# Performance work log

Hardware: AMD Instinct MI355X
Metric: run time of the kernel (lower is better)

## Reference

```python
import heapq
import jax, jax.numpy as jnp
import numpy as np

NB_CLASSES = 50257
INPUT_DIM = 512
BATCH = 1024
NB_REQ = 8


def build_huffman(nb_classes):
    """Replicates Huffmax.build: huffman tree over equal frequencies,
    codes padded with 0, paths padded with root node id."""
    heap = [(1, i, i) for i in range(nb_classes)]  # (freq, tiebreak, payload)
    heapq.heapify(heap)
    node_id = 0
    tiebreak = nb_classes
    while len(heap) > 1:
        f1, _, left = heapq.heappop(heap)
        f2, _, right = heapq.heappop(heap)
        heapq.heappush(heap, (f1 + f2, tiebreak, ('n', node_id, left, right)))
        node_id += 1
        tiebreak += 1
    root = heap[0][2]
    total_nodes = node_id  # = nb_classes - 1
    root_id = root[1]
    codes, paths = {}, {}
    stack = [(root, [], [])]
    while stack:
        node, code, path = stack.pop()
        if isinstance(node, tuple):
            _, nid, l, r = node
            stack.append((l, code + [0], path + [nid]))
            stack.append((r, code + [1], path + [nid]))
        else:
            codes[node] = code
            paths[node] = path
    max_depth = max(len(c) for c in codes.values())
    code_arr = np.zeros((nb_classes, max_depth), np.float32)
    path_arr = np.full((nb_classes, max_depth), root_id, np.int32)
    for c in range(nb_classes):
        code_arr[c, :len(codes[c])] = codes[c]
        path_arr[c, :len(paths[c])] = paths[c]
    return code_arr, path_arr, total_nodes


def setup_inputs() -> dict:
    key = jax.random.key(0)
    k1, k2, k3 = jax.random.split(key, 3)
    code_arr, path_arr, total_nodes = build_huffman(NB_CLASSES)
    input_vector = jax.random.normal(k1, (BATCH, INPUT_DIM), dtype=jnp.float32)
    target_classes = jax.random.randint(k2, (BATCH, NB_REQ), 0, NB_CLASSES, dtype=jnp.int32)
    # glorot-ish scaled node weights (original W is (total_nodes, input_dim, 1))
    W = jax.random.normal(k3, (total_nodes, INPUT_DIM), dtype=jnp.float32) * (1.0 / np.sqrt(INPUT_DIM))
    b = jnp.zeros((total_nodes,), dtype=jnp.float32)
    return {
        'input_vector': input_vector,
        'target_classes': target_classes,
        'W': W,
        'b': b,
        'class_paths': jnp.asarray(path_arr),
        'huffman_codes': jnp.asarray(code_arr),
    }


def reference(input_vector, target_classes, W, b, class_paths, huffman_codes):
    # req_nodes: (B, R, D) node ids along huffman path for each requested class
    req_nodes = class_paths[target_classes]
    # req_W: (B, R, D, I) gathered node weight rows; y = x . W_node + b_node
    req_W = W[req_nodes]
    y = jnp.einsum('bi,brdi->brd', input_vector, req_W) + b[req_nodes]
    y = jax.nn.sigmoid(y)
    codes = huffman_codes[target_classes]  # (B, R, D) in {0,1} (0-padded)
    # factor = y if code==0 else (1-y); product along the path
    return jnp.prod(codes + y - 2.0 * codes * y, axis=-1)
```

## Files before the change

### kernel.cpp

```cpp
#include <hip/hip_runtime.h>
#include <math.h>

template<int CTRL, int ROW_MASK>
__device__ __forceinline__ float dpp_add(float v) {
    const int s = __builtin_amdgcn_update_dpp(0, __float_as_int(v),
                                              CTRL, ROW_MASK, 0xf, false);
    return v + __int_as_float(s);
}

__device__ __forceinline__ float wave_sum63(float v) {
    v = dpp_add<0x111, 0xf>(v);
    v = dpp_add<0x112, 0xf>(v);
    v = dpp_add<0x114, 0xf>(v);
    v = dpp_add<0x118, 0xf>(v);
    v = dpp_add<0x142, 0xa>(v);
    v = dpp_add<0x143, 0xc>(v);
    return v;
}

__device__ __forceinline__ float readlane_f(float v, int l) {
    return __int_as_float(__builtin_amdgcn_readlane(__float_as_int(v), l));
}

__global__ __launch_bounds__(256, 4)
void huff_half(const float* __restrict__ x, const int* __restrict__ tgt,
               const float* __restrict__ W, const float* __restrict__ bias,
               const int* __restrict__ paths, const float* __restrict__ codes,
               float* __restrict__ out, int R, int I)
{
    __shared__ float qsh[2][2];
    const int lane = threadIdx.x & 63;
    const int w    = threadIdx.x >> 6;
    const int pi   = w >> 1;
    const int h    = w & 1;
    const int p    = blockIdx.x * 2 + pi;
    const int b    = p / R;

    const float4* xrow = reinterpret_cast<const float4*>(x + (size_t)b * I);
    const float4 xa = xrow[lane];
    const float4 xb = xrow[lane + 64];

    const int c     = tgt[p];
    const int dglob = h * 8 + (lane & 7);
    const int   nd = paths[(size_t)c * 16 + dglob];
    const float cd = codes[(size_t)c * 16 + dglob];
    const float sd = 1.0f - 2.0f * cd;
    const float bv = bias[nd];

    float acc[8];
    #pragma unroll
    for (int d = 0; d < 8; ++d) {
        const int nid = __builtin_amdgcn_readlane(nd, d);
        const float4* wr = reinterpret_cast<const float4*>(W + (size_t)nid * I);
        const float4 wa = wr[lane];
        const float4 wb = wr[lane + 64];
        acc[d] = xa.x * wa.x + xa.y * wa.y + xa.z * wa.z + xa.w * wa.w
               + xb.x * wb.x + xb.y * wb.y + xb.z * wb.z + xb.w * wb.w;
    }

    #pragma unroll
    for (int d = 0; d < 8; ++d) acc[d] = wave_sum63(acc[d]);

    float q = 1.0f;
    #pragma unroll
    for (int d = 0; d < 8; ++d) {
        const float tot = readlane_f(acc[d], 63);
        const float bb  = readlane_f(bv, d);
        const float ss  = readlane_f(sd, d);
        q *= 1.0f + __expf(-ss * (tot + bb));
    }
    if (lane == 0) qsh[pi][h] = q;
    __syncthreads();
    if (h == 0 && lane == 0) out[p] = 1.0f / (qsh[pi][0] * qsh[pi][1]);
}

__global__ __launch_bounds__(256)
void huff_kernel_gen(const float* __restrict__ x, const int* __restrict__ tgt,
                     const float* __restrict__ W, const float* __restrict__ bias,
                     const int* __restrict__ paths, const float* __restrict__ codes,
                     float* __restrict__ out, int R, int I, int D, int npairs)
{
    const int lane = threadIdx.x & 63;
    const int p = blockIdx.x * 4 + (threadIdx.x >> 6);
    if (p >= npairs) return;
    const int b = p / R;
    const float4* xrow = reinterpret_cast<const float4*>(x + (size_t)b * I);
    const float4 xa = xrow[lane];
    const float4 xb = xrow[lane + 64];
    const int c = tgt[p];
    float q = 1.0f;
    for (int d = 0; d < D; ++d) {
        const int node = paths[(size_t)c * D + d];
        const float4* wr = reinterpret_cast<const float4*>(W + (size_t)node * I);
        const float4 wa = wr[lane];
        const float4 wb = wr[lane + 64];
        float acc = xa.x * wa.x + xa.y * wa.y + xa.z * wa.z + xa.w * wa.w
                  + xb.x * wb.x + xb.y * wb.y + xb.z * wb.z + xb.w * wb.w;
        #pragma unroll
        for (int off = 32; off; off >>= 1) acc += __shfl_xor(acc, off, 64);
        const float t = acc + bias[node];
        const float s = 1.0f - 2.0f * codes[(size_t)c * D + d];
        q *= 1.0f + __expf(-s * t);
    }
    if (lane == 0) out[p] = 1.0f / q;
}

extern "C" void kernel_launch(void* const* d_in, const int* in_sizes, int n_in,
                              void* d_out, int out_size, void* d_ws, size_t ws_size,
                              hipStream_t stream) {
    const float* x     = (const float*)d_in[0];
    const int*   tgt   = (const int*)  d_in[1];
    const float* W     = (const float*)d_in[2];
    const float* bias  = (const float*)d_in[3];
    const int*   paths = (const int*)  d_in[4];
    const float* codes = (const float*)d_in[5];
    float* out = (float*)d_out;

    const int N = in_sizes[3];
    const int C = N + 1;
    const int I = in_sizes[2] / N;
    const int B = in_sizes[0] / I;
    const int R = in_sizes[1] / B;
    const int D = in_sizes[4] / C;

    const int npairs = B * R;

    if (D == 16 && I == 512 && (npairs & 1) == 0) {
        huff_half<<<npairs / 2, 256, 0, stream>>>(x, tgt, W, bias, paths, codes,
                                                  out, R, I);
    } else {
        const int grid = (npairs + 3) / 4;
        huff_kernel_gen<<<grid, 256, 0, stream>>>(x, tgt, W, bias, paths, codes,
                                                  out, R, I, D, npairs);
    }
}
```

Before: 24.12 us.

## Precompute top-tree node logits densely, gather remaining path nodes per pair

Adds a dense pre-pass that computes logits for the top 128 Huffman nodes (highest ids, near the root) for every batch row into workspace. The per-pair kernel then reads the first seven shared path nodes from that table and only gathers and dots the remaining nine weight rows. A fallback loop handles pairs whose first seven nodes are not all in the table. This trades redundant per-pair gathers of heavily shared upper-tree rows for an extra launch, a workspace round trip, and reliance on the node-id layout of the tree construction.

```diff
diff --git a/kernel.cpp b/kernel.cpp
--- a/kernel.cpp
+++ b/kernel.cpp
@@ -1,13 +1,18 @@
 #include <hip/hip_runtime.h>
 #include <math.h>
 
+#define TOPM 128
+
 template<int CTRL, int ROW_MASK>
 __device__ __forceinline__ float dpp_add(float v) {
-    const int s = __builtin_amdgcn_update_dpp(0, __float_as_int(v),
-                                              CTRL, ROW_MASK, 0xf, false);
+    const int s = __builtin_amdgcn_update_dpp(0, __float_as_int(v), CTRL, ROW_MASK, 0xf, false);
     return v + __int_as_float(s);
 }
-
+template<int CTRL, int ROW_MASK>
+__device__ __forceinline__ float dpp_mul(float v) {
+    const int s = __builtin_amdgcn_update_dpp(0x3f800000, __float_as_int(v), CTRL, ROW_MASK, 0xf, false);
+    return v * __int_as_float(s);
+}
 __device__ __forceinline__ float wave_sum63(float v) {
     v = dpp_add<0x111, 0xf>(v);
     v = dpp_add<0x112, 0xf>(v);
@@ -17,61 +22,134 @@
     v = dpp_add<0x143, 0xc>(v);
     return v;
 }
-
+__device__ __forceinline__ float wave_prod63(float v) {
+    v = dpp_mul<0x111, 0xf>(v);
+    v = dpp_mul<0x112, 0xf>(v);
+    v = dpp_mul<0x114, 0xf>(v);
+    v = dpp_mul<0x118, 0xf>(v);
+    v = dpp_mul<0x142, 0xa>(v);
+    v = dpp_mul<0x143, 0xc>(v);
+    return v;
+}
 __device__ __forceinline__ float readlane_f(float v, int l) {
     return __int_as_float(__builtin_amdgcn_readlane(__float_as_int(v), l));
 }
-
-__global__ __launch_bounds__(256, 4)
-void huff_half(const float* __restrict__ x, const int* __restrict__ tgt,
-               const float* __restrict__ W, const float* __restrict__ bias,
-               const int* __restrict__ paths, const float* __restrict__ codes,
-               float* __restrict__ out, int R, int I)
+__device__ __forceinline__ float dot8(float4 a, float4 b, float4 c, float4 d) {
+    return a.x*b.x + a.y*b.y + a.z*b.z + a.w*b.w
+         + c.x*d.x + c.y*d.y + c.z*d.z + c.w*d.w;
+}
+
+__global__ __launch_bounds__(256)
+void dense_top(const float* __restrict__ x, const float* __restrict__ W,
+               const float* __restrict__ bias, float* __restrict__ ytop, int N)
 {
-    __shared__ float qsh[2][2];
     const int lane = threadIdx.x & 63;
-    const int w    = threadIdx.x >> 6;
-    const int pi   = w >> 1;
-    const int h    = w & 1;
-    const int p    = blockIdx.x * 2 + pi;
-    const int b    = p / R;
-
-    const float4* xrow = reinterpret_cast<const float4*>(x + (size_t)b * I);
-    const float4 xa = xrow[lane];
-    const float4 xb = xrow[lane + 64];
-
-    const int c     = tgt[p];
-    const int dglob = h * 8 + (lane & 7);
-    const int   nd = paths[(size_t)c * 16 + dglob];
-    const float cd = codes[(size_t)c * 16 + dglob];
+    const int wi = blockIdx.x * 4 + (threadIdx.x >> 6);
+    const int bchunk = wi >> 4;
+    const int jg = wi & 15;
+    const int tb = N - TOPM;
+
+    float4 wa[8], wb[8];
+    #pragma unroll
+    for (int r = 0; r < 8; ++r) {
+        const float4* wr = reinterpret_cast<const float4*>(W + (size_t)(tb + jg*8 + r) * 512);
+        wa[r] = wr[lane]; wb[r] = wr[lane + 64];
+    }
+    float bb[8];
+    #pragma unroll
+    for (int r = 0; r < 8; ++r) bb[r] = bias[tb + jg*8 + r];
+
+    for (int bl = 0; bl < 16; ++bl) {
+        const int b = bchunk * 16 + bl;
+        const float4* xr = reinterpret_cast<const float4*>(x + (size_t)b * 512);
+        const float4 xa = xr[lane], xb = xr[lane + 64];
+        float acc[8];
+        #pragma unroll
+        for (int r = 0; r < 8; ++r) acc[r] = dot8(xa, wa[r], xb, wb[r]);
+        #pragma unroll
+        for (int r = 0; r < 8; ++r) acc[r] = wave_sum63(acc[r]);
+        float tv = 0.0f;
+        #pragma unroll
+        for (int r = 0; r < 8; ++r) {
+            const float tot = readlane_f(acc[r], 63) + bb[r];
+            tv = (lane == r) ? tot : tv;
+        }
+        if (lane < 8) ytop[(size_t)b * TOPM + jg * 8 + lane] = tv;
+    }
+}
+
+__global__ __launch_bounds__(256)
+void huff_table(const float* __restrict__ x, const int* __restrict__ tgt,
+                const float* __restrict__ W, const float* __restrict__ bias,
+                const int* __restrict__ paths, const float* __restrict__ codes,
+                const float* __restrict__ ytop, float* __restrict__ out,
+                int R, int N)
+{
+    const int lane = threadIdx.x & 63;
+    const int p = blockIdx.x * 4 + (threadIdx.x >> 6);
+    const int b = p / R;
+    const int tb = N - TOPM;
+
+    const float4* xr = reinterpret_cast<const float4*>(x + (size_t)b * 512);
+    const float4 xa = xr[lane], xb = xr[lane + 64];
+
+    const int c = tgt[p];
+    const int dd = (lane < 16) ? lane : 15;
+    const int   nd = paths[(size_t)c * 16 + dd];
+    const float cd = codes[(size_t)c * 16 + dd];
     const float sd = 1.0f - 2.0f * cd;
     const float bv = bias[nd];
 
-    float acc[8];
-    #pragma unroll
-    for (int d = 0; d < 8; ++d) {
-        const int nid = __builtin_amdgcn_readlane(nd, d);
-        const float4* wr = reinterpret_cast<const float4*>(W + (size_t)nid * I);
-        const float4 wa = wr[lane];
-        const float4 wb = wr[lane + 64];
-        acc[d] = xa.x * wa.x + xa.y * wa.y + xa.z * wa.z + xa.w * wa.w
-               + xb.x * wb.x + xb.y * wb.y + xb.z * wb.z + xb.w * wb.w;
-    }
-
-    #pragma unroll
-    for (int d = 0; d < 8; ++d) acc[d] = wave_sum63(acc[d]);
-
-    float q = 1.0f;
-    #pragma unroll
-    for (int d = 0; d < 8; ++d) {
-        const float tot = readlane_f(acc[d], 63);
-        const float bb  = readlane_f(bv, d);
-        const float ss  = readlane_f(sd, d);
-        q *= 1.0f + __expf(-ss * (tot + bb));
-    }
-    if (lane == 0) qsh[pi][h] = q;
-    __syncthreads();
-    if (h == 0 && lane == 0) out[p] = 1.0f / (qsh[pi][0] * qsh[pi][1]);
+    const unsigned long long gmask = __ballot(lane < 16 && nd < tb);
+
+    if ((gmask & 0x7Full) == 0) {
+        float tval = 0.0f;
+        if (lane < 7) tval = ytop[(size_t)b * TOPM + (nd - tb)];
+
+        float4 wA[9], wB[9];
+        #pragma unroll
+        for (int i = 0; i < 9; ++i) {
+            const int snid = __builtin_amdgcn_readlane(nd, 7 + i);
+            const float4* wr = reinterpret_cast<const float4*>(W + (size_t)snid * 512);
+            wA[i] = wr[lane]; wB[i] = wr[lane + 64];
+        }
+        float acc[9];
+        #pragma unroll
+        for (int i = 0; i < 9; ++i) acc[i] = dot8(xa, wA[i], xb, wB[i]);
+        #pragma unroll
+        for (int i = 0; i < 9; ++i) acc[i] = wave_sum63(acc[i]);
+
+        float f = 1.0f;
+        if (lane < 7) f = 1.0f + __expf(-sd * tval);
+        f = wave_prod63(f);
+        float q = readlane_f(f, 63);
+
+        #pragma unroll
+        for (int i = 0; i < 9; ++i) {
+            const float tot = readlane_f(acc[i], 63) + readlane_f(bv, 7 + i);
+            const float ss  = readlane_f(sd, 7 + i);
+            q *= 1.0f + __expf(-ss * tot);
+        }
+        if (lane == 0) out[p] = 1.0f / q;
+    } else {
+        float q = 1.0f;
+        for (int d = 0; d < 16; ++d) {
+            const int snid = __builtin_amdgcn_readlane(nd, d);
+            const float ss = readlane_f(sd, d);
+            float t;
+            if (snid >= tb) {
+                t = ytop[(size_t)b * TOPM + (snid - tb)];
+            } else {
+                const float4* wr = reinterpret_cast<const float4*>(W + (size_t)snid * 512);
+                const float4 wva = wr[lane], wvb = wr[lane + 64];
+                float a = dot8(xa, wva, xb, wvb);
+                a = wave_sum63(a);
+                t = readlane_f(a, 63) + readlane_f(bv, d);
+            }
+            q *= 1.0f + __expf(-ss * t);
+        }
+        if (lane == 0) out[p] = 1.0f / q;
+    }
 }
 
 __global__ __launch_bounds__(256)
@@ -94,8 +172,7 @@
         const float4* wr = reinterpret_cast<const float4*>(W + (size_t)node * I);
         const float4 wa = wr[lane];
         const float4 wb = wr[lane + 64];
-        float acc = xa.x * wa.x + xa.y * wa.y + xa.z * wa.z + xa.w * wa.w
-                  + xb.x * wb.x + xb.y * wb.y + xb.z * wb.z + xb.w * wb.w;
+        float acc = dot8(xa, wa, xb, wb);
         #pragma unroll
         for (int off = 32; off; off >>= 1) acc += __shfl_xor(acc, off, 64);
         const float t = acc + bias[node];
@@ -124,10 +201,14 @@
     const int D = in_sizes[4] / C;
 
     const int npairs = B * R;
-
-    if (D == 16 && I == 512 && (npairs & 1) == 0) {
-        huff_half<<<npairs / 2, 256, 0, stream>>>(x, tgt, W, bias, paths, codes,
-                                                  out, R, I);
+    const size_t ws_need = (size_t)B * TOPM * sizeof(float);
+
+    if (D == 16 && I == 512 && (B % 16) == 0 && (npairs % 4) == 0 &&
+        N > TOPM && ws_size >= ws_need) {
+        float* ytop = (float*)d_ws;
+        dense_top<<<B / 4, 256, 0, stream>>>(x, W, bias, ytop, N);
+        huff_table<<<npairs / 4, 256, 0, stream>>>(x, tgt, W, bias, paths, codes,
+                                                   ytop, out, R, N);
     } else {
         const int grid = (npairs + 3) / 4;
         huff_kernel_gen<<<grid, 256, 0, stream>>>(x, tgt, W, bias, paths, codes,
```

Result: slower. 35.27 us (+46.2%).
